# Kernel tuning notes

Measured on AMD Instinct MI355X. Metric: run time of the kernel, lower is better.

Reference implementation:

```python
import jax, jax.numpy as jnp
import numpy as np

N = 8192
NFEAT = 512
NHID = 256
NCLASS = 40
EDGE_P = 0.002  # ~16 avg degree


def setup_inputs() -> dict:
    key = jax.random.key(0)
    k1, k2, k3, k4 = jax.random.split(key, 4)
    x = jax.random.normal(k1, (N, NFEAT), dtype=jnp.float32)
    # unnormalized binary adjacency without self loops (module adds eye itself)
    adj = (jax.random.uniform(k2, (N, N)) < EDGE_P).astype(jnp.float32)
    # GCNConv weights: torch.rand(in, out) -> uniform[0,1)
    W1 = jax.random.uniform(k3, (NFEAT, NHID), dtype=jnp.float32)
    W2 = jax.random.uniform(k4, (NHID, NCLASS), dtype=jnp.float32)
    return {"x": x, "adj": adj, "W1": W1, "W2": W2}


def reference(x, adj, W1, W2):
    n = adj.shape[0]
    # add self loops: in_adj.to_dense() + eye
    A_hat = adj + jnp.eye(n, dtype=adj.dtype)
    # normalize_adj: D^{-1/2} A_hat D^{-1/2} (diag matmuls == row/col scaling)
    d = A_hat.sum(-1) ** -0.5  # [N]
    norm_adj = d[:, None] * A_hat * d[None, :]
    # conv1: relu(adj @ x @ W1); dropout is identity in eval mode
    h = jax.nn.relu((norm_adj @ x) @ W1)
    # conv2 reuses the same normalized adjacency (only one DGG layer by default)
    h2 = jax.nn.relu((norm_adj @ h) @ W2)
    return jax.nn.log_softmax(h2, axis=-1)
```

## Files before the change

kernel.cpp:

```cpp
#include <hip/hip_runtime.h>
#include <math.h>

#define NV 8192
#define CAP 64

typedef __attribute__((ext_vector_type(8))) short short8;
typedef __attribute__((ext_vector_type(4))) float f32x4;

static __device__ __forceinline__ unsigned short f2bf(float v) {
  unsigned int u = __float_as_uint(v);
  unsigned int r = (u + 0x7fffu + ((u >> 16) & 1u)) >> 16;
  return (unsigned short)r;
}
static __device__ __forceinline__ float bf2f(unsigned short h) {
  return __uint_as_float(((unsigned int)h) << 16);
}

__global__ __launch_bounds__(256) void mega_build_gemm1(
    const float* __restrict__ adj, const float* __restrict__ x,
    const float* __restrict__ W1, int* __restrict__ cols,
    int* __restrict__ rowcount, float* __restrict__ dinv,
    float* __restrict__ diagv, float* __restrict__ XW1) {
  __shared__ __align__(16) unsigned short sAh[64][40];
  __shared__ __align__(16) unsigned short sAl[64][40];
  __shared__ __align__(16) unsigned short sBh[64][40];
  __shared__ __align__(16) unsigned short sBl[64][40];
  __shared__ int cnt;
  __shared__ int diag_nz;

  int t = threadIdx.x;
  int lane = t & 63;

  if (blockIdx.x < 512) {
    const int K = 512;
    int b = blockIdx.x;
    int bn = (b & 3) * 64;
    int bm = (b >> 2) * 64;
    int w = t >> 6;
    int quad = lane >> 4, m16 = lane & 15;
    f32x4 acc[4] = {};
    for (int k0 = 0; k0 < K; k0 += 32) {
#pragma unroll
      for (int i = 0; i < 2; i++) {
        int id = t + i * 256;
        int row = id >> 3;
        int fq = id & 7;
        float4 v = *(const float4*)&x[(size_t)(bm + row) * K + k0 + fq * 4];
        ushort4 h, l;
        h.x = f2bf(v.x); l.x = f2bf(v.x - bf2f(h.x));
        h.y = f2bf(v.y); l.y = f2bf(v.y - bf2f(h.y));
        h.z = f2bf(v.z); l.z = f2bf(v.z - bf2f(h.z));
        h.w = f2bf(v.w); l.w = f2bf(v.w - bf2f(h.w));
        *(ushort4*)&sAh[row][fq * 4] = h;
        *(ushort4*)&sAl[row][fq * 4] = l;
      }
#pragma unroll
      for (int j = 0; j < 2; j++) {
        int id = t + j * 256;
        int k = id >> 4;
        int n4 = (id & 15) * 4;
        float4 v = *(const float4*)&W1[(size_t)(k0 + k) * 256 + bn + n4];
        float va[4] = {v.x, v.y, v.z, v.w};
#pragma unroll
        for (int c = 0; c < 4; c++) {
          unsigned short h = f2bf(va[c]);
          sBh[n4 + c][k] = h;
          sBl[n4 + c][k] = f2bf(va[c] - bf2f(h));
        }
      }
      __syncthreads();
      short8 ah = *(const short8*)&sAh[w * 16 + m16][quad * 8];
      short8 al = *(const short8*)&sAl[w * 16 + m16][quad * 8];
#pragma unroll
      for (int j = 0; j < 4; j++) {
        short8 bh = *(const short8*)&sBh[j * 16 + m16][quad * 8];
        short8 bl = *(const short8*)&sBl[j * 16 + m16][quad * 8];
        acc[j] = __builtin_amdgcn_mfma_f32_16x16x32_bf16(ah, bh, acc[j], 0, 0, 0);
        acc[j] = __builtin_amdgcn_mfma_f32_16x16x32_bf16(al, bh, acc[j], 0, 0, 0);
        acc[j] = __builtin_amdgcn_mfma_f32_16x16x32_bf16(ah, bl, acc[j], 0, 0, 0);
      }
      __syncthreads();
    }
#pragma unroll
    for (int j = 0; j < 4; j++)
#pragma unroll
      for (int r = 0; r < 4; r++)
        XW1[(size_t)(bm + w * 16 + quad * 4 + r) * 256 + bn + j * 16 + m16] =
            acc[j][r];
  } else {
    int row = blockIdx.x - 512;
    if (t == 0) { cnt = 0; diag_nz = 0; }
    __syncthreads();
    const float4* arow = (const float4*)(adj + (size_t)row * NV);
    float4 vv[8];
    vv[0] = arow[t + 0 * 256];
    vv[1] = arow[t + 1 * 256];
    vv[2] = arow[t + 2 * 256];
    vv[3] = arow[t + 3 * 256];
    vv[4] = arow[t + 4 * 256];
    vv[5] = arow[t + 5 * 256];
    vv[6] = arow[t + 6 * 256];
    vv[7] = arow[t + 7 * 256];
    unsigned int wm = 0;
#pragma unroll
    for (int u = 0; u < 8; u++) {
      float va[4] = {vv[u].x, vv[u].y, vv[u].z, vv[u].w};
#pragma unroll
      for (int j = 0; j < 4; j++) {
        bool nz = (va[j] != 0.0f);
        int c = 4 * t + (u << 10) + j;
        if (nz) {
          if (c == row) diag_nz = 1;
          else wm |= 1u << (u * 4 + j);
        }
      }
    }
    int myc = __popc(wm);
    int pre = myc;
#pragma unroll
    for (int off = 1; off < 64; off <<= 1) {
      int nb = __shfl_up(pre, off, 64);
      if (lane >= off) pre += nb;
    }
    int wtot = __shfl(pre, 63, 64);
    int base = 0;
    if (lane == 63) base = atomicAdd(&cnt, wtot);
    base = __shfl(base, 63, 64);
    int p0 = base + (pre - myc);
    while (wm) {
      int p = __ffs(wm) - 1;
      wm &= wm - 1;
      int c = 4 * t + ((p >> 2) << 10) + (p & 3);
      if (p0 < CAP) cols[(size_t)row * CAP + p0] = c;
      p0++;
    }
    __syncthreads();
    if (t == 0) {
      float deg = (float)(cnt + diag_nz) + 1.0f;
      dinv[row] = 1.0f / sqrtf(deg);
      diagv[row] = diag_nz ? 2.0f : 1.0f;
      rowcount[row] = cnt > CAP ? CAP : cnt;
    }
  }
}

__global__ __launch_bounds__(256) void spmm_relu_k(
    const float* __restrict__ Z, const int* __restrict__ cols,
    const int* __restrict__ rowcount, const float* __restrict__ dinv,
    const float* __restrict__ diagv, float* __restrict__ H) {
  int lane = threadIdx.x & 63;
  int row = blockIdx.x * 4 + (threadIdx.x >> 6);
  const float4* Zr = (const float4*)Z;
  float di = dinv[row];
  float4 z = Zr[(size_t)row * 64 + lane];
  float dd = diagv[row] * di;
  float4 acc;
  acc.x = dd * z.x; acc.y = dd * z.y; acc.z = dd * z.z; acc.w = dd * z.w;
  int cnt = rowcount[row];
  const int* cr = cols + (size_t)row * CAP;
  int e = 0;
  for (; e + 8 <= cnt; e += 8) {
    int c0 = cr[e + 0], c1 = cr[e + 1], c2 = cr[e + 2], c3 = cr[e + 3];
    int c4 = cr[e + 4], c5 = cr[e + 5], c6 = cr[e + 6], c7 = cr[e + 7];
    float w0 = dinv[c0], w1 = dinv[c1], w2 = dinv[c2], w3 = dinv[c3];
    float w4 = dinv[c4], w5 = dinv[c5], w6 = dinv[c6], w7 = dinv[c7];
    float4 g0 = Zr[(size_t)c0 * 64 + lane];
    float4 g1 = Zr[(size_t)c1 * 64 + lane];
    float4 g2 = Zr[(size_t)c2 * 64 + lane];
    float4 g3 = Zr[(size_t)c3 * 64 + lane];
    float4 g4 = Zr[(size_t)c4 * 64 + lane];
    float4 g5 = Zr[(size_t)c5 * 64 + lane];
    float4 g6 = Zr[(size_t)c6 * 64 + lane];
    float4 g7 = Zr[(size_t)c7 * 64 + lane];
    acc.x += w0 * g0.x + w1 * g1.x + w2 * g2.x + w3 * g3.x;
    acc.y += w0 * g0.y + w1 * g1.y + w2 * g2.y + w3 * g3.y;
    acc.z += w0 * g0.z + w1 * g1.z + w2 * g2.z + w3 * g3.z;
    acc.w += w0 * g0.w + w1 * g1.w + w2 * g2.w + w3 * g3.w;
    acc.x += w4 * g4.x + w5 * g5.x + w6 * g6.x + w7 * g7.x;
    acc.y += w4 * g4.y + w5 * g5.y + w6 * g6.y + w7 * g7.y;
    acc.z += w4 * g4.z + w5 * g5.z + w6 * g6.z + w7 * g7.z;
    acc.w += w4 * g4.w + w5 * g5.w + w6 * g6.w + w7 * g7.w;
  }
  for (; e + 4 <= cnt; e += 4) {
    int c0 = cr[e + 0], c1 = cr[e + 1], c2 = cr[e + 2], c3 = cr[e + 3];
    float w0 = dinv[c0], w1 = dinv[c1], w2 = dinv[c2], w3 = dinv[c3];
    float4 g0 = Zr[(size_t)c0 * 64 + lane];
    float4 g1 = Zr[(size_t)c1 * 64 + lane];
    float4 g2 = Zr[(size_t)c2 * 64 + lane];
    float4 g3 = Zr[(size_t)c3 * 64 + lane];
    acc.x += w0 * g0.x + w1 * g1.x + w2 * g2.x + w3 * g3.x;
    acc.y += w0 * g0.y + w1 * g1.y + w2 * g2.y + w3 * g3.y;
    acc.z += w0 * g0.z + w1 * g1.z + w2 * g2.z + w3 * g3.z;
    acc.w += w0 * g0.w + w1 * g1.w + w2 * g2.w + w3 * g3.w;
  }
  for (; e < cnt; e++) {
    int c = cr[e];
    float w = dinv[c];
    float4 g = Zr[(size_t)c * 64 + lane];
    acc.x += w * g.x; acc.y += w * g.y; acc.z += w * g.z; acc.w += w * g.w;
  }
  float4 o;
  o.x = fmaxf(acc.x * di, 0.0f);
  o.y = fmaxf(acc.y * di, 0.0f);
  o.z = fmaxf(acc.z * di, 0.0f);
  o.w = fmaxf(acc.w * di, 0.0f);
  ((float4*)H)[(size_t)row * 64 + lane] = o;
}

__global__ __launch_bounds__(256) void gemm2_mfma(
    const float* __restrict__ H, const float* __restrict__ W2,
    float* __restrict__ HW2) {
  const int K = 256;
  __shared__ __align__(16) unsigned short sAh[32][40];
  __shared__ __align__(16) unsigned short sAl[32][40];
  __shared__ __align__(16) unsigned short sBh[64][40];
  __shared__ __align__(16) unsigned short sBl[64][40];
  int t = threadIdx.x;
  int bm = blockIdx.x * 32;
  int lane = t & 63, w = t >> 6;
  int quad = lane >> 4, m16 = lane & 15;
  int i = w & 1;
  int jj = (w >> 1) * 2;
  f32x4 acc[2] = {};
  for (int k0 = 0; k0 < K; k0 += 32) {
    {
      int row = t >> 3;
      int fq = t & 7;
      float4 v = *(const float4*)&H[(size_t)(bm + row) * K + k0 + fq * 4];
      ushort4 h, l;
      h.x = f2bf(v.x); l.x = f2bf(v.x - bf2f(h.x));
      h.y = f2bf(v.y); l.y = f2bf(v.y - bf2f(h.y));
      h.z = f2bf(v.z); l.z = f2bf(v.z - bf2f(h.z));
      h.w = f2bf(v.w); l.w = f2bf(v.w - bf2f(h.w));
      *(ushort4*)&sAh[row][fq * 4] = h;
      *(ushort4*)&sAl[row][fq * 4] = l;
    }
#pragma unroll
    for (int j = 0; j < 2; j++) {
      int id = t + j * 256;
      int k = id >> 4;
      int n4 = (id & 15) * 4;
#pragma unroll
      for (int c = 0; c < 4; c++) {
        float v = (n4 + c < 40) ? W2[(size_t)(k0 + k) * 40 + n4 + c] : 0.0f;
        unsigned short h = f2bf(v);
        sBh[n4 + c][k] = h;
        sBl[n4 + c][k] = f2bf(v - bf2f(h));
      }
    }
    __syncthreads();
    short8 ah = *(const short8*)&sAh[i * 16 + m16][quad * 8];
    short8 al = *(const short8*)&sAl[i * 16 + m16][quad * 8];
#pragma unroll
    for (int jx = 0; jx < 2; jx++) {
      short8 bh = *(const short8*)&sBh[(jj + jx) * 16 + m16][quad * 8];
      short8 bl = *(const short8*)&sBl[(jj + jx) * 16 + m16][quad * 8];
      acc[jx] = __builtin_amdgcn_mfma_f32_16x16x32_bf16(ah, bh, acc[jx], 0, 0, 0);
      acc[jx] = __builtin_amdgcn_mfma_f32_16x16x32_bf16(al, bh, acc[jx], 0, 0, 0);
      acc[jx] = __builtin_amdgcn_mfma_f32_16x16x32_bf16(ah, bl, acc[jx], 0, 0, 0);
    }
    __syncthreads();
  }
#pragma unroll
  for (int jx = 0; jx < 2; jx++)
#pragma unroll
    for (int r = 0; r < 4; r++)
      HW2[(size_t)(bm + i * 16 + quad * 4 + r) * 64 + (jj + jx) * 16 + m16] =
          acc[jx][r];
}

__global__ __launch_bounds__(256) void spmm2_lsm_k(
    const float* __restrict__ Z, const int* __restrict__ cols,
    const int* __restrict__ rowcount, const float* __restrict__ dinv,
    const float* __restrict__ diagv, float* __restrict__ out) {
  int lane = threadIdx.x & 63;
  int row = blockIdx.x * 4 + (threadIdx.x >> 6);
  float di = dinv[row];
  float acc = diagv[row] * di * Z[(size_t)row * 64 + lane];
  int cnt = rowcount[row];
  const int* cr = cols + (size_t)row * CAP;
  int e = 0;
  for (; e + 8 <= cnt; e += 8) {
    int c0 = cr[e + 0], c1 = cr[e + 1], c2 = cr[e + 2], c3 = cr[e + 3];
    int c4 = cr[e + 4], c5 = cr[e + 5], c6 = cr[e + 6], c7 = cr[e + 7];
    float w0 = dinv[c0], w1 = dinv[c1], w2 = dinv[c2], w3 = dinv[c3];
    float w4 = dinv[c4], w5 = dinv[c5], w6 = dinv[c6], w7 = dinv[c7];
    float g0 = Z[(size_t)c0 * 64 + lane];
    float g1 = Z[(size_t)c1 * 64 + lane];
    float g2 = Z[(size_t)c2 * 64 + lane];
    float g3 = Z[(size_t)c3 * 64 + lane];
    float g4 = Z[(size_t)c4 * 64 + lane];
    float g5 = Z[(size_t)c5 * 64 + lane];
    float g6 = Z[(size_t)c6 * 64 + lane];
    float g7 = Z[(size_t)c7 * 64 + lane];
    acc += w0 * g0 + w1 * g1 + w2 * g2 + w3 * g3;
    acc += w4 * g4 + w5 * g5 + w6 * g6 + w7 * g7;
  }
  for (; e + 4 <= cnt; e += 4) {
    int c0 = cr[e + 0], c1 = cr[e + 1], c2 = cr[e + 2], c3 = cr[e + 3];
    float w0 = dinv[c0], w1 = dinv[c1], w2 = dinv[c2], w3 = dinv[c3];
    acc += w0 * Z[(size_t)c0 * 64 + lane] + w1 * Z[(size_t)c1 * 64 + lane] +
           w2 * Z[(size_t)c2 * 64 + lane] + w3 * Z[(size_t)c3 * 64 + lane];
  }
  for (; e < cnt; e++) {
    int c = cr[e];
    acc += dinv[c] * Z[(size_t)c * 64 + lane];
  }
  float h2 = (lane < 40) ? fmaxf(acc * di, 0.0f) : -INFINITY;
  float m = h2;
  for (int off = 32; off > 0; off >>= 1) m = fmaxf(m, __shfl_xor(m, off, 64));
  float ex = (lane < 40) ? expf(h2 - m) : 0.0f;
  float s = ex;
  for (int off = 32; off > 0; off >>= 1) s += __shfl_xor(s, off, 64);
  float ls = logf(s);
  if (lane < 40) out[(size_t)row * 40 + lane] = h2 - m - ls;
}

extern "C" void kernel_launch(void* const* d_in, const int* in_sizes, int n_in,
                              void* d_out, int out_size, void* d_ws, size_t ws_size,
                              hipStream_t stream) {
  (void)in_sizes; (void)n_in; (void)out_size; (void)ws_size;
  const float* x   = (const float*)d_in[0];
  const float* adj = (const float*)d_in[1];
  const float* W1  = (const float*)d_in[2];
  const float* W2  = (const float*)d_in[3];
  float* out = (float*)d_out;
  char* ws = (char*)d_ws;

  int*   cols     = (int*)(ws);
  int*   rowcount = (int*)(ws + 2097152);
  float* dinv     = (float*)(ws + 2129920);
  float* diagv    = (float*)(ws + 2162688);
  float* XW1      = (float*)(ws + 2195456);
  float* H        = (float*)(ws + 10584064);
  float* HW2      = (float*)(ws + 18972672);

  hipLaunchKernelGGL(mega_build_gemm1, dim3(512 + NV), dim3(256), 0, stream,
                     adj, x, W1, cols, rowcount, dinv, diagv, XW1);
  hipLaunchKernelGGL(spmm_relu_k, dim3(NV / 4), dim3(256), 0, stream,
                     XW1, cols, rowcount, dinv, diagv, H);
  hipLaunchKernelGGL(gemm2_mfma, dim3(NV / 32), dim3(256), 0, stream,
                     H, W2, HW2);
  hipLaunchKernelGGL(spmm2_lsm_k, dim3(NV / 4), dim3(256), 0, stream,
                     HW2, cols, rowcount, dinv, diagv, out);
}
```

Baseline: 407.5 us.

## Fuse first sparse aggregation with second GEMM via shared-memory H tile

Merges the SpMM+ReLU kernel and the W2 GEMM into one kernel. Each 512-thread block aggregates 32 rows of XW1 into a shared-memory tile, then runs split-bf16 MFMA against W2 directly from LDS. This drops the global H round trip (8 MB written and read back) and one launch. In exchange the grid shrinks from 2048 to 256 blocks, which lowers latency hiding for the gather, and each wave now re-reads and re-converts W2 from global memory every k step.

```diff
diff --git a/kernel.cpp b/kernel.cpp
--- a/kernel.cpp
+++ b/kernel.cpp
@@ -144,129 +144,113 @@
   }
 }
 
-__global__ __launch_bounds__(256) void spmm_relu_k(
-    const float* __restrict__ Z, const int* __restrict__ cols,
+__global__ __launch_bounds__(512) void spmm1_gemm2_k(
+    const float* __restrict__ XW1, const int* __restrict__ cols,
     const int* __restrict__ rowcount, const float* __restrict__ dinv,
-    const float* __restrict__ diagv, float* __restrict__ H) {
-  int lane = threadIdx.x & 63;
-  int row = blockIdx.x * 4 + (threadIdx.x >> 6);
-  const float4* Zr = (const float4*)Z;
-  float di = dinv[row];
-  float4 z = Zr[(size_t)row * 64 + lane];
-  float dd = diagv[row] * di;
-  float4 acc;
-  acc.x = dd * z.x; acc.y = dd * z.y; acc.z = dd * z.z; acc.w = dd * z.w;
-  int cnt = rowcount[row];
-  const int* cr = cols + (size_t)row * CAP;
-  int e = 0;
-  for (; e + 8 <= cnt; e += 8) {
-    int c0 = cr[e + 0], c1 = cr[e + 1], c2 = cr[e + 2], c3 = cr[e + 3];
-    int c4 = cr[e + 4], c5 = cr[e + 5], c6 = cr[e + 6], c7 = cr[e + 7];
-    float w0 = dinv[c0], w1 = dinv[c1], w2 = dinv[c2], w3 = dinv[c3];
-    float w4 = dinv[c4], w5 = dinv[c5], w6 = dinv[c6], w7 = dinv[c7];
-    float4 g0 = Zr[(size_t)c0 * 64 + lane];
-    float4 g1 = Zr[(size_t)c1 * 64 + lane];
-    float4 g2 = Zr[(size_t)c2 * 64 + lane];
-    float4 g3 = Zr[(size_t)c3 * 64 + lane];
-    float4 g4 = Zr[(size_t)c4 * 64 + lane];
-    float4 g5 = Zr[(size_t)c5 * 64 + lane];
-    float4 g6 = Zr[(size_t)c6 * 64 + lane];
-    float4 g7 = Zr[(size_t)c7 * 64 + lane];
-    acc.x += w0 * g0.x + w1 * g1.x + w2 * g2.x + w3 * g3.x;
-    acc.y += w0 * g0.y + w1 * g1.y + w2 * g2.y + w3 * g3.y;
-    acc.z += w0 * g0.z + w1 * g1.z + w2 * g2.z + w3 * g3.z;
-    acc.w += w0 * g0.w + w1 * g1.w + w2 * g2.w + w3 * g3.w;
-    acc.x += w4 * g4.x + w5 * g5.x + w6 * g6.x + w7 * g7.x;
-    acc.y += w4 * g4.y + w5 * g5.y + w6 * g6.y + w7 * g7.y;
-    acc.z += w4 * g4.z + w5 * g5.z + w6 * g6.z + w7 * g7.z;
-    acc.w += w4 * g4.w + w5 * g5.w + w6 * g6.w + w7 * g7.w;
-  }
-  for (; e + 4 <= cnt; e += 4) {
-    int c0 = cr[e + 0], c1 = cr[e + 1], c2 = cr[e + 2], c3 = cr[e + 3];
-    float w0 = dinv[c0], w1 = dinv[c1], w2 = dinv[c2], w3 = dinv[c3];
-    float4 g0 = Zr[(size_t)c0 * 64 + lane];
-    float4 g1 = Zr[(size_t)c1 * 64 + lane];
-    float4 g2 = Zr[(size_t)c2 * 64 + lane];
-    float4 g3 = Zr[(size_t)c3 * 64 + lane];
-    acc.x += w0 * g0.x + w1 * g1.x + w2 * g2.x + w3 * g3.x;
-    acc.y += w0 * g0.y + w1 * g1.y + w2 * g2.y + w3 * g3.y;
-    acc.z += w0 * g0.z + w1 * g1.z + w2 * g2.z + w3 * g3.z;
-    acc.w += w0 * g0.w + w1 * g1.w + w2 * g2.w + w3 * g3.w;
-  }
-  for (; e < cnt; e++) {
-    int c = cr[e];
-    float w = dinv[c];
-    float4 g = Zr[(size_t)c * 64 + lane];
-    acc.x += w * g.x; acc.y += w * g.y; acc.z += w * g.z; acc.w += w * g.w;
-  }
-  float4 o;
-  o.x = fmaxf(acc.x * di, 0.0f);
-  o.y = fmaxf(acc.y * di, 0.0f);
-  o.z = fmaxf(acc.z * di, 0.0f);
-  o.w = fmaxf(acc.w * di, 0.0f);
-  ((float4*)H)[(size_t)row * 64 + lane] = o;
-}
-
-__global__ __launch_bounds__(256) void gemm2_mfma(
-    const float* __restrict__ H, const float* __restrict__ W2,
+    const float* __restrict__ diagv, const float* __restrict__ W2,
     float* __restrict__ HW2) {
-  const int K = 256;
-  __shared__ __align__(16) unsigned short sAh[32][40];
-  __shared__ __align__(16) unsigned short sAl[32][40];
-  __shared__ __align__(16) unsigned short sBh[64][40];
-  __shared__ __align__(16) unsigned short sBl[64][40];
+  __shared__ __align__(16) float sH[32][260];
   int t = threadIdx.x;
+  int lane = t & 63;
+  int w = t >> 6;
   int bm = blockIdx.x * 32;
-  int lane = t & 63, w = t >> 6;
+  const float4* Zr = (const float4*)XW1;
+
+#pragma unroll
+  for (int pass = 0; pass < 4; pass++) {
+    int r = pass * 8 + w;
+    int row = bm + r;
+    float di = dinv[row];
+    float4 z = Zr[(size_t)row * 64 + lane];
+    float dd = diagv[row] * di;
+    float4 acc;
+    acc.x = dd * z.x; acc.y = dd * z.y; acc.z = dd * z.z; acc.w = dd * z.w;
+    int cnt = rowcount[row];
+    const int* cr = cols + (size_t)row * CAP;
+    int e = 0;
+    for (; e + 8 <= cnt; e += 8) {
+      int c0 = cr[e + 0], c1 = cr[e + 1], c2 = cr[e + 2], c3 = cr[e + 3];
+      int c4 = cr[e + 4], c5 = cr[e + 5], c6 = cr[e + 6], c7 = cr[e + 7];
+      float w0 = dinv[c0], w1 = dinv[c1], w2 = dinv[c2], w3 = dinv[c3];
+      float w4 = dinv[c4], w5 = dinv[c5], w6 = dinv[c6], w7 = dinv[c7];
+      float4 g0 = Zr[(size_t)c0 * 64 + lane];
+      float4 g1 = Zr[(size_t)c1 * 64 + lane];
+      float4 g2 = Zr[(size_t)c2 * 64 + lane];
+      float4 g3 = Zr[(size_t)c3 * 64 + lane];
+      float4 g4 = Zr[(size_t)c4 * 64 + lane];
+      float4 g5 = Zr[(size_t)c5 * 64 + lane];
+      float4 g6 = Zr[(size_t)c6 * 64 + lane];
+      float4 g7 = Zr[(size_t)c7 * 64 + lane];
+      acc.x += w0 * g0.x + w1 * g1.x + w2 * g2.x + w3 * g3.x;
+      acc.y += w0 * g0.y + w1 * g1.y + w2 * g2.y + w3 * g3.y;
+      acc.z += w0 * g0.z + w1 * g1.z + w2 * g2.z + w3 * g3.z;
+      acc.w += w0 * g0.w + w1 * g1.w + w2 * g2.w + w3 * g3.w;
+      acc.x += w4 * g4.x + w5 * g5.x + w6 * g6.x + w7 * g7.x;
+      acc.y += w4 * g4.y + w5 * g5.y + w6 * g6.y + w7 * g7.y;
+      acc.z += w4 * g4.z + w5 * g5.z + w6 * g6.z + w7 * g7.z;
+      acc.w += w4 * g4.w + w5 * g5.w + w6 * g6.w + w7 * g7.w;
+    }
+    for (; e + 4 <= cnt; e += 4) {
+      int c0 = cr[e + 0], c1 = cr[e + 1], c2 = cr[e + 2], c3 = cr[e + 3];
+      float w0 = dinv[c0], w1 = dinv[c1], w2 = dinv[c2], w3 = dinv[c3];
+      float4 g0 = Zr[(size_t)c0 * 64 + lane];
+      float4 g1 = Zr[(size_t)c1 * 64 + lane];
+      float4 g2 = Zr[(size_t)c2 * 64 + lane];
+      float4 g3 = Zr[(size_t)c3 * 64 + lane];
+      acc.x += w0 * g0.x + w1 * g1.x + w2 * g2.x + w3 * g3.x;
+      acc.y += w0 * g0.y + w1 * g1.y + w2 * g2.y + w3 * g3.y;
+      acc.z += w0 * g0.z + w1 * g1.z + w2 * g2.z + w3 * g3.z;
+      acc.w += w0 * g0.w + w1 * g1.w + w2 * g2.w + w3 * g3.w;
+    }
+    for (; e < cnt; e++) {
+      int c = cr[e];
+      float ww = dinv[c];
+      float4 g = Zr[(size_t)c * 64 + lane];
+      acc.x += ww * g.x; acc.y += ww * g.y; acc.z += ww * g.z; acc.w += ww * g.w;
+    }
+    float4 o;
+    o.x = fmaxf(acc.x * di, 0.0f);
+    o.y = fmaxf(acc.y * di, 0.0f);
+    o.z = fmaxf(acc.z * di, 0.0f);
+    o.w = fmaxf(acc.w * di, 0.0f);
+    *(float4*)&sH[r][lane * 4] = o;
+  }
+  __syncthreads();
+
   int quad = lane >> 4, m16 = lane & 15;
   int i = w & 1;
-  int jj = (w >> 1) * 2;
-  f32x4 acc[2] = {};
-  for (int k0 = 0; k0 < K; k0 += 32) {
-    {
-      int row = t >> 3;
-      int fq = t & 7;
-      float4 v = *(const float4*)&H[(size_t)(bm + row) * K + k0 + fq * 4];
-      ushort4 h, l;
-      h.x = f2bf(v.x); l.x = f2bf(v.x - bf2f(h.x));
-      h.y = f2bf(v.y); l.y = f2bf(v.y - bf2f(h.y));
-      h.z = f2bf(v.z); l.z = f2bf(v.z - bf2f(h.z));
-      h.w = f2bf(v.w); l.w = f2bf(v.w - bf2f(h.w));
-      *(ushort4*)&sAh[row][fq * 4] = h;
-      *(ushort4*)&sAl[row][fq * 4] = l;
-    }
-#pragma unroll
-    for (int j = 0; j < 2; j++) {
-      int id = t + j * 256;
-      int k = id >> 4;
-      int n4 = (id & 15) * 4;
-#pragma unroll
-      for (int c = 0; c < 4; c++) {
-        float v = (n4 + c < 40) ? W2[(size_t)(k0 + k) * 40 + n4 + c] : 0.0f;
+  int j = w >> 1;
+  int n = j * 16 + m16;
+  int rl = i * 16 + m16;
+  f32x4 acc2 = {};
+  for (int k0 = 0; k0 < 256; k0 += 32) {
+    short8 bh = {}, bl = {};
+    if (n < 40) {
+#pragma unroll
+      for (int e2 = 0; e2 < 8; e2++) {
+        float v = W2[(size_t)(k0 + quad * 8 + e2) * 40 + n];
         unsigned short h = f2bf(v);
-        sBh[n4 + c][k] = h;
-        sBl[n4 + c][k] = f2bf(v - bf2f(h));
-      }
-    }
-    __syncthreads();
-    short8 ah = *(const short8*)&sAh[i * 16 + m16][quad * 8];
-    short8 al = *(const short8*)&sAl[i * 16 + m16][quad * 8];
-#pragma unroll
-    for (int jx = 0; jx < 2; jx++) {
-      short8 bh = *(const short8*)&sBh[(jj + jx) * 16 + m16][quad * 8];
-      short8 bl = *(const short8*)&sBl[(jj + jx) * 16 + m16][quad * 8];
-      acc[jx] = __builtin_amdgcn_mfma_f32_16x16x32_bf16(ah, bh, acc[jx], 0, 0, 0);
-      acc[jx] = __builtin_amdgcn_mfma_f32_16x16x32_bf16(al, bh, acc[jx], 0, 0, 0);
-      acc[jx] = __builtin_amdgcn_mfma_f32_16x16x32_bf16(ah, bl, acc[jx], 0, 0, 0);
-    }
-    __syncthreads();
-  }
-#pragma unroll
-  for (int jx = 0; jx < 2; jx++)
-#pragma unroll
-    for (int r = 0; r < 4; r++)
-      HW2[(size_t)(bm + i * 16 + quad * 4 + r) * 64 + (jj + jx) * 16 + m16] =
-          acc[jx][r];
+        bh[e2] = (short)h;
+        bl[e2] = (short)f2bf(v - bf2f(h));
+      }
+    }
+    float4 a0 = *(const float4*)&sH[rl][k0 + quad * 8];
+    float4 a1 = *(const float4*)&sH[rl][k0 + quad * 8 + 4];
+    float af[8] = {a0.x, a0.y, a0.z, a0.w, a1.x, a1.y, a1.z, a1.w};
+    short8 ah, al;
+#pragma unroll
+    for (int e2 = 0; e2 < 8; e2++) {
+      unsigned short h = f2bf(af[e2]);
+      ah[e2] = (short)h;
+      al[e2] = (short)f2bf(af[e2] - bf2f(h));
+    }
+    acc2 = __builtin_amdgcn_mfma_f32_16x16x32_bf16(ah, bh, acc2, 0, 0, 0);
+    acc2 = __builtin_amdgcn_mfma_f32_16x16x32_bf16(al, bh, acc2, 0, 0, 0);
+    acc2 = __builtin_amdgcn_mfma_f32_16x16x32_bf16(ah, bl, acc2, 0, 0, 0);
+  }
+#pragma unroll
+  for (int r = 0; r < 4; r++)
+    HW2[(size_t)(bm + i * 16 + quad * 4 + r) * 64 + n] = acc2[r];
 }
 
 __global__ __launch_bounds__(256) void spmm2_lsm_k(
@@ -332,15 +316,12 @@
   float* dinv     = (float*)(ws + 2129920);
   float* diagv    = (float*)(ws + 2162688);
   float* XW1      = (float*)(ws + 2195456);
-  float* H        = (float*)(ws + 10584064);
-  float* HW2      = (float*)(ws + 18972672);
+  float* HW2      = (float*)(ws + 10584064);
 
   hipLaunchKernelGGL(mega_build_gemm1, dim3(512 + NV), dim3(256), 0, stream,
                      adj, x, W1, cols, rowcount, dinv, diagv, XW1);
-  hipLaunchKernelGGL(spmm_relu_k, dim3(NV / 4), dim3(256), 0, stream,
-                     XW1, cols, rowcount, dinv, diagv, H);
-  hipLaunchKernelGGL(gemm2_mfma, dim3(NV / 32), dim3(256), 0, stream,
-                     H, W2, HW2);
+  hipLaunchKernelGGL(spmm1_gemm2_k, dim3(NV / 32), dim3(512), 0, stream,
+                     XW1, cols, rowcount, dinv, diagv, W2, HW2);
   hipLaunchKernelGGL(spmm2_lsm_k, dim3(NV / 4), dim3(256), 0, stream,
                      HW2, cols, rowcount, dinv, diagv, out);
 }
```

Measured after the change: 399.4 us. 1.02x faster.
